# Performance work log

Measured on AMD Instinct MI355X. Metric: run time of the kernel, lower is better.

Reference implementation:

```python
import jax, jax.numpy as jnp
import numpy as np

B, S, D = 2, 2048, 2048
NH, NKV, HD = 16, 4, 128
REP = NH // NKV
EPS = 1e-6
ROPE_THETA = 1e6


def setup_inputs() -> dict:
    key = jax.random.key(0)
    ks = jax.random.split(key, 6)
    x = jax.random.normal(ks[0], (B, S, D), jnp.float32)
    # real rotary embeddings: [S, HD]
    inv_freq = 1.0 / (ROPE_THETA ** (np.arange(0, HD, 2, dtype=np.float64) / HD))
    freqs = np.outer(np.arange(S, dtype=np.float64), inv_freq)
    emb = np.concatenate([freqs, freqs], axis=-1)
    cos = jnp.asarray(np.cos(emb), jnp.float32)
    sin = jnp.asarray(np.sin(emb), jnp.float32)
    scale = 1.0 / np.sqrt(D)
    Wq = jax.random.normal(ks[1], (D, NH * HD), jnp.float32) * scale   # [in, out]
    Wk = jax.random.normal(ks[2], (D, NKV * HD), jnp.float32) * scale
    Wv = jax.random.normal(ks[3], (D, NKV * HD), jnp.float32) * scale
    Wo = jax.random.normal(ks[4], (NH * HD, D), jnp.float32) * (1.0 / np.sqrt(NH * HD))
    q_norm_w = jnp.ones((HD,), jnp.float32)
    k_norm_w = jnp.ones((HD,), jnp.float32)
    return dict(x=x, cos=cos, sin=sin, Wq=Wq, Wk=Wk, Wv=Wv, Wo=Wo,
                q_norm_w=q_norm_w, k_norm_w=k_norm_w)


def _rms_norm(h, w):
    var = jnp.mean(h * h, axis=-1, keepdims=True)
    return w * (h * jax.lax.rsqrt(var + EPS))


def _rotate_half(h):
    h1, h2 = jnp.split(h, 2, axis=-1)
    return jnp.concatenate([-h2, h1], axis=-1)


def reference(x, cos, sin, Wq, Wk, Wv, Wo, q_norm_w, k_norm_w):
    b, s, _ = x.shape
    q = (x @ Wq).reshape(b, s, NH, HD)
    k = (x @ Wk).reshape(b, s, NKV, HD)
    v = (x @ Wv).reshape(b, s, NKV, HD)
    # per-head QK RMSNorm
    q = _rms_norm(q, q_norm_w)
    k = _rms_norm(k, k_norm_w)
    # RoPE: cos/sin [S,HD] -> broadcast over batch and heads
    c = cos[None, :, None, :]
    s_ = sin[None, :, None, :]
    q = q * c + _rotate_half(q) * s_
    k = k * c + _rotate_half(k) * s_
    # GQA: group q heads per kv head instead of materializing repeat_kv
    qg = q.reshape(b, s, NKV, REP, HD)
    scores = jnp.einsum('bqgrd,bkgd->bgrqk', qg, k) / np.sqrt(HD)
    causal = jnp.tril(jnp.ones((s, s), bool))  # [q,k]
    scores = jnp.where(causal, scores, -jnp.inf)
    probs = jax.nn.softmax(scores.astype(jnp.float32), axis=-1).astype(q.dtype)
    out = jnp.einsum('bgrqk,bkgd->bqgrd', probs, v).reshape(b, s, NH * HD)
    return out @ Wo
```

## Files before the change

kernel.cpp:

```cpp
#include <hip/hip_runtime.h>
#include <hip/hip_bf16.h>
#include <math.h>

#define B_ 2
#define S_ 2048
#define D_ 2048
#define NH_ 16
#define NKV_ 4
#define HD_ 128
#define EPS_ 1e-6f
#define SCALE_ 0.08838834764831845f
#define LOG2E_ 1.4426950408889634f
#define KOFF_ 2048
#define VOFF_ 2560

typedef float f32x4 __attribute__((ext_vector_type(4)));
typedef short bf16x8 __attribute__((ext_vector_type(8)));
typedef short short4v __attribute__((ext_vector_type(4)));
typedef float float4v __attribute__((ext_vector_type(4)));
typedef unsigned uint2v __attribute__((ext_vector_type(2)));
typedef unsigned uint4v __attribute__((ext_vector_type(4)));

static __device__ __forceinline__ short f2bf(float f) {
    union { float f; unsigned u; } x{f};
    unsigned r = (x.u + 0x7fff + ((x.u >> 16) & 1)) >> 16;
    return (short)r;
}
static __device__ __forceinline__ float bf2f(short s) {
    union { unsigned u; float f; } x; x.u = ((unsigned)(unsigned short)s) << 16; return x.f;
}
static __device__ __forceinline__ unsigned pack_bf2(float a, float b) {
    return __builtin_amdgcn_perm(__builtin_bit_cast(unsigned, b),
                                 __builtin_bit_cast(unsigned, a), 0x07060302u);
}

#define AS1(p) ((const __attribute__((address_space(1))) void*)(p))
#define AS3(p) ((__attribute__((address_space(3))) void*)(p))
static __device__ __forceinline__ void async16(const void* g, void* l) {
    __builtin_amdgcn_global_load_lds(AS1(g), AS3(l), 16, 0, 0);
}
#define SB_() __builtin_amdgcn_sched_barrier(0)

__global__ __launch_bounds__(256) void cast_kernel(const float* __restrict__ in,
                                                   short* __restrict__ out) {
    size_t i = ((size_t)blockIdx.x * 256 + threadIdx.x) * 4;
    float4v v = *(const float4v*)(in + i);
    short4v o; o.x = f2bf(v.x); o.y = f2bf(v.y); o.z = f2bf(v.z); o.w = f2bf(v.w);
    *(short4v*)(out + i) = o;
}

__global__ __launch_bounds__(256) void transpose_all_kernel(const float* __restrict__ Wq,
                                                            const float* __restrict__ Wk,
                                                            const float* __restrict__ Wv,
                                                            const float* __restrict__ Wo,
                                                            short* __restrict__ Wt,
                                                            short* __restrict__ Wot) {
    __shared__ float tile[64][65];
    const int bx = blockIdx.x, by = blockIdx.y;
    const float* src; short* dst; int N, nb;
    if (bx < 32)      { src = Wq; dst = Wt;                         N = 2048; nb = bx; }
    else if (bx < 40) { src = Wk; dst = Wt + (size_t)KOFF_ * 2048;  N = 512;  nb = bx - 32; }
    else if (bx < 48) { src = Wv; dst = Wt + (size_t)VOFF_ * 2048;  N = 512;  nb = bx - 40; }
    else              { src = Wo; dst = Wot;                        N = 2048; nb = bx - 48; }
    const int n0 = nb * 64, k0 = by * 64;
    const int tid = threadIdx.x;
    for (int r = 0; r < 16; ++r) {
        int k = r * 4 + (tid >> 6);
        int n = tid & 63;
        tile[k][n] = src[(size_t)(k0 + k) * N + n0 + n];
    }
    __syncthreads();
    for (int r = 0; r < 4; ++r) {
        int n  = r * 16 + (tid >> 4);
        int kk = (tid & 15) * 4;
        short4v o4;
        o4.x = f2bf(tile[kk + 0][n]); o4.y = f2bf(tile[kk + 1][n]);
        o4.z = f2bf(tile[kk + 2][n]); o4.w = f2bf(tile[kk + 3][n]);
        *(short4v*)&dst[(size_t)(n0 + n) * 2048 + k0 + kk] = o4;
    }
}

__global__ __launch_bounds__(512, 2) void gemm_oproj_kernel(const short* __restrict__ A,
                                                            const short* __restrict__ Bt,
                                                            float* __restrict__ C) {
    __shared__ __align__(16) short smem[49152];
    short* A0 = smem;
    short* A1 = smem + 8192;
    short* B0 = smem + 16384;
    short* B1 = smem + 32768;

    const int tid  = threadIdx.x;
    const int orig = blockIdx.y * 8 + blockIdx.x;
    const int swz  = (orig & 7) * 32 + (orig >> 3);
    const int bn = swz & 7, bm = swz >> 3;
    const int wave = tid >> 6, lane = tid & 63;
    const int quad = lane >> 4, l16 = lane & 15;
    const int wr = wave >> 2, wc = wave & 3;

    const short* Ag = A  + (size_t)(bm * 128) * 2048;
    const short* Bg = Bt + (size_t)(bn * 256) * 2048;

    f32x4 acc[4][4];
#pragma unroll
    for (int i = 0; i < 4; ++i)
#pragma unroll
        for (int j = 0; j < 4; ++j) acc[i][j] = (f32x4){0.f, 0.f, 0.f, 0.f};

    bf16x8 a[4][2], b0[2][2], b1[2][2];

    auto stage_half = [&](const short* gpanel, int t, int h, short* lslot) {
#pragma unroll
        for (int u = 0; u < 2; ++u) {
            int ci = u * 512 + tid;
            int r  = ci >> 3;
            int cb = ((ci & 7) * 16) ^ ((r & 7) << 4);
            async16(gpanel + (size_t)(h * 128 + r) * 2048 + t * 64 + (cb >> 1),
                    lslot + h * 8192 + ci * 8);
        }
    };

#define OLDA_(lbuf) \
    _Pragma("unroll") for (int mt = 0; mt < 4; ++mt) \
    _Pragma("unroll") for (int ks = 0; ks < 2; ++ks) { \
        int row_ = wr * 64 + mt * 16 + l16; \
        int cb_  = (ks * 64 + quad * 16) ^ ((row_ & 7) << 4); \
        a[mt][ks] = *(const bf16x8*)&(lbuf)[row_ * 64 + (cb_ >> 1)]; \
    }
#define OLDB_(lbuf, qn, breg) \
    _Pragma("unroll") for (int ntl = 0; ntl < 2; ++ntl) \
    _Pragma("unroll") for (int ks = 0; ks < 2; ++ks) { \
        int row_ = wc * 64 + (qn) * 32 + ntl * 16 + l16; \
        int cb_  = (ks * 64 + quad * 16) ^ ((row_ & 7) << 4); \
        breg[ntl][ks] = *(const bf16x8*)&(lbuf)[row_ * 64 + (cb_ >> 1)]; \
    }
#define OBAR_() do { SB_(); __builtin_amdgcn_s_barrier(); } while (0)
#define OMFMA_(qn, breg) do { \
    __builtin_amdgcn_s_setprio(1); \
    _Pragma("unroll") for (int mt = 0; mt < 4; ++mt) \
    _Pragma("unroll") for (int ntl = 0; ntl < 2; ++ntl) \
    _Pragma("unroll") for (int ks = 0; ks < 2; ++ks) \
        acc[mt][(qn) * 2 + ntl] = __builtin_amdgcn_mfma_f32_16x16x32_bf16( \
            a[mt][ks], breg[ntl][ks], acc[mt][(qn) * 2 + ntl], 0, 0, 0); \
    __builtin_amdgcn_s_setprio(0); SB_(); __builtin_amdgcn_s_barrier(); } while (0)

    stage_half(Bg, 0, 0, B0); stage_half(Bg, 0, 1, B0);
    stage_half(Ag, 0, 0, A0);
    SB_(); asm volatile("s_waitcnt vmcnt(0)" ::: "memory");
    __builtin_amdgcn_s_barrier();

#pragma unroll 1
    for (int i = 0; i < 16; ++i) {
        const int tE = 2 * i, tO = 2 * i + 1;
        const bool more = (i < 15);

        stage_half(Ag, tO, 0, A1);
        stage_half(Bg, tO, 0, B1); stage_half(Bg, tO, 1, B1);
        OLDA_(A0); OLDB_(B0, 0, b0);
        OBAR_();
        OMFMA_(0, b0);

        if (more) {
            stage_half(Ag, tE + 2, 0, A0);
            SB_(); asm volatile("s_waitcnt vmcnt(2)" ::: "memory");
        } else {
            SB_(); asm volatile("s_waitcnt vmcnt(0)" ::: "memory");
        }
        OLDB_(B0, 1, b1);
        OBAR_();
        OMFMA_(1, b1);

        if (more) { stage_half(Bg, tE + 2, 0, B0); stage_half(Bg, tE + 2, 1, B0); }
        OLDA_(A1); OLDB_(B1, 0, b0);
        OBAR_();
        OMFMA_(0, b0);

        if (more) { SB_(); asm volatile("s_waitcnt vmcnt(0)" ::: "memory"); }
        OLDB_(B1, 1, b1);
        OBAR_();
        OMFMA_(1, b1);
    }

#pragma unroll
    for (int mt = 0; mt < 4; ++mt)
#pragma unroll
        for (int nt = 0; nt < 4; ++nt)
#pragma unroll
            for (int j = 0; j < 4; ++j) {
                int row = bm * 128 + wr * 64 + mt * 16 + quad * 4 + j;
                int col = bn * 256 + wc * 64 + nt * 16 + l16;
                C[(size_t)row * 2048 + col] = acc[mt][nt][j];
            }
#undef OLDA_
#undef OLDB_
#undef OBAR_
#undef OMFMA_
}

#define QKV_ITERS 16

__global__ __launch_bounds__(512, 2) void qkv_fused_kernel(const short* __restrict__ xb,
                                                           const short* __restrict__ Wt,
                                                           const float* __restrict__ cosb,
                                                           const float* __restrict__ sinb,
                                                           const float* __restrict__ qw,
                                                           const float* __restrict__ kw,
                                                           short* __restrict__ q_rope,
                                                           short* __restrict__ k_rope,
                                                           short* __restrict__ vtr) {
    __shared__ __align__(16) short smem[65536];
    __shared__ float ss2[4][256];

    short* A0 = smem;
    short* A1 = smem + 16384;
    short* B0 = smem + 32768;
    short* B1 = smem + 49152;

    const int tid  = threadIdx.x;
    const int orig = blockIdx.y * 12 + blockIdx.x;
    const int swz  = (orig & 7) * 24 + (orig >> 3);
    const int bn = swz % 12, bm = swz / 12;
    const int wave = tid >> 6, lane = tid & 63;
    const int quad = lane >> 4, l16 = lane & 15;
    const int wr = wave >> 2, wc = wave & 3;

    const short* Ag = xb + (size_t)(bm * 256) * 2048;
    const short* Bg = Wt + (size_t)(bn * 256) * 2048;

    f32x4 acc[8][4];
#pragma unroll
    for (int i = 0; i < 8; ++i)
#pragma unroll
        for (int j = 0; j < 4; ++j) acc[i][j] = (f32x4){0.f, 0.f, 0.f, 0.f};

    bf16x8 a[4][2], b0[2][2], b1[2][2];

    auto stage_half = [&](const short* gpanel, int t, int h, short* lslot) {
#pragma unroll
        for (int u = 0; u < 2; ++u) {
            int ci = u * 512 + tid;
            int r  = ci >> 3;
            int cb = ((ci & 7) * 16) ^ ((r & 7) << 4);
            async16(gpanel + (size_t)(h * 128 + r) * 2048 + t * 64 + (cb >> 1),
                    lslot + h * 8192 + ci * 8);
        }
    };

#define LDA_(lbuf, qm) \
    _Pragma("unroll") for (int mt = 0; mt < 4; ++mt) \
    _Pragma("unroll") for (int ks = 0; ks < 2; ++ks) { \
        int row_ = wr * 128 + (qm) * 64 + mt * 16 + l16; \
        int cb_  = (ks * 64 + quad * 16) ^ ((row_ & 7) << 4); \
        a[mt][ks] = *(const bf16x8*)&(lbuf)[row_ * 64 + (cb_ >> 1)]; \
    }
#define LDB_(lbuf, qn, breg) \
    _Pragma("unroll") for (int ntl = 0; ntl < 2; ++ntl) \
    _Pragma("unroll") for (int ks = 0; ks < 2; ++ks) { \
        int row_ = wc * 64 + (qn) * 32 + ntl * 16 + l16; \
        int cb_  = (ks * 64 + quad * 16) ^ ((row_ & 7) << 4); \
        breg[ntl][ks] = *(const bf16x8*)&(lbuf)[row_ * 64 + (cb_ >> 1)]; \
    }
#define MFMA16_(qm, qn, breg) \
    _Pragma("unroll") for (int mt = 0; mt < 4; ++mt) \
    _Pragma("unroll") for (int ntl = 0; ntl < 2; ++ntl) \
    _Pragma("unroll") for (int ks = 0; ks < 2; ++ks) \
        acc[(qm) * 4 + mt][(qn) * 2 + ntl] = __builtin_amdgcn_mfma_f32_16x16x32_bf16( \
            a[mt][ks], breg[ntl][ks], acc[(qm) * 4 + mt][(qn) * 2 + ntl], 0, 0, 0);
#define PH_BAR() do { __builtin_amdgcn_sched_barrier(0); __builtin_amdgcn_s_barrier(); } while (0)
#define PH_MFMA2(qm) do { \
        __builtin_amdgcn_s_setprio(1); MFMA16_(qm, 0, b0); MFMA16_(qm, 1, b1); \
        __builtin_amdgcn_s_setprio(0); \
        __builtin_amdgcn_sched_barrier(0); __builtin_amdgcn_s_barrier(); } while (0)

    stage_half(Bg, 0, 0, B0); stage_half(Bg, 0, 1, B0);
    stage_half(Ag, 0, 0, A0); stage_half(Ag, 0, 1, A0);
    stage_half(Bg, 1, 0, B1); stage_half(Bg, 1, 1, B1);
    asm volatile("s_waitcnt vmcnt(4)" ::: "memory");
    __builtin_amdgcn_s_barrier();

#pragma unroll 1
    for (int i = 0; i < QKV_ITERS; ++i) {
        const int tE = 2 * i, tO = 2 * i + 1;
        const bool more = (i < QKV_ITERS - 1);

        LDA_(A0, 0); LDB_(B0, 0, b0); LDB_(B0, 1, b1);
        stage_half(Ag, tO, 0, A1); stage_half(Ag, tO, 1, A1);
        PH_BAR();
        PH_MFMA2(0);

        LDA_(A0, 1);
        if (more) {
            stage_half(Bg, tE + 2, 0, B0); stage_half(Bg, tE + 2, 1, B0);
            asm volatile("s_waitcnt vmcnt(4)" ::: "memory");
        } else {
            asm volatile("s_waitcnt vmcnt(0)" ::: "memory");
        }
        PH_BAR();
        PH_MFMA2(1);

        LDA_(A1, 0); LDB_(B1, 0, b0); LDB_(B1, 1, b1);
        if (more) { stage_half(Ag, tE + 2, 0, A0); stage_half(Ag, tE + 2, 1, A0); }
        PH_BAR();
        PH_MFMA2(0);

        LDA_(A1, 1);
        if (more) {
            stage_half(Bg, tO + 2, 0, B1); stage_half(Bg, tO + 2, 1, B1);
            asm volatile("s_waitcnt vmcnt(4)" ::: "memory");
        }
        PH_BAR();
        PH_MFMA2(1);
    }

    if (bn >= 10) {
        const int gbase = (bn - 10) * 2;
#pragma unroll
        for (int am = 0; am < 8; ++am) {
            int tok0 = bm * 256 + wr * 128 + am * 16 + quad * 4;
            int bb = tok0 >> 11, s0 = tok0 & (S_ - 1);
#pragma unroll
            for (int nt = 0; nt < 4; ++nt) {
                int col = wc * 64 + nt * 16 + l16;
                int g = gbase + (col >> 7);
                int d = col & 127;
                short4v o4;
                o4.x = f2bf(acc[am][nt][0]); o4.y = f2bf(acc[am][nt][1]);
                o4.z = f2bf(acc[am][nt][2]); o4.w = f2bf(acc[am][nt][3]);
                *(short4v*)&vtr[((size_t)(bb * NKV_ + g) * HD_ + d) * S_ + s0] = o4;
            }
        }
        return;
    }

    {
        float pss[8][4];
#pragma unroll
        for (int am = 0; am < 8; ++am)
#pragma unroll
            for (int j = 0; j < 4; ++j) {
                float s = 0.f;
#pragma unroll
                for (int nt = 0; nt < 4; ++nt) s += acc[am][nt][j] * acc[am][nt][j];
                pss[am][j] = s;
            }
#pragma unroll
        for (int off = 1; off < 16; off <<= 1)
#pragma unroll
            for (int am = 0; am < 8; ++am)
#pragma unroll
                for (int j = 0; j < 4; ++j)
                    pss[am][j] += __shfl_xor(pss[am][j], off);
        if (l16 == 0)
#pragma unroll
            for (int am = 0; am < 8; ++am)
#pragma unroll
                for (int j = 0; j < 4; ++j)
                    ss2[wc][wr * 128 + am * 16 + quad * 4 + j] = pss[am][j];
    }
    short* ct = smem;
#pragma unroll
    for (int am = 0; am < 8; ++am)
#pragma unroll
        for (int nt = 0; nt < 4; ++nt)
#pragma unroll
            for (int j = 0; j < 4; ++j)
                ct[(wr * 128 + am * 16 + quad * 4 + j) * 256 + wc * 64 + nt * 16 + l16]
                    = f2bf(acc[am][nt][j]);
    __syncthreads();

    const bool isQ = (bn < 8);
    const float osc = isQ ? (SCALE_ * LOG2E_) : 1.0f;
    const float* w = isQ ? qw : kw;
#pragma unroll 1
    for (int it = 0; it < 16; ++it) {
        int idx = it * 512 + tid;
        int row = idx >> 5;
        int s32 = idx & 31;
        int head = s32 >> 4, seg = s32 & 15;
        int tok = bm * 256 + row;
        int bb = tok >> 11, s = tok & (S_ - 1);
        float rstd = rsqrtf((ss2[2 * head][row] + ss2[2 * head + 1][row]) * (1.0f / HD_) + EPS_);
        int c0 = seg * 8, p0 = (seg ^ 8) * 8;
        bf16x8 ta = *(const bf16x8*)&ct[row * 256 + head * 128 + c0];
        bf16x8 tb = *(const bf16x8*)&ct[row * 256 + head * 128 + p0];
        float sgn = (seg < 8) ? -1.0f : 1.0f;
        float4v cs0 = *(const float4v*)&cosb[(size_t)s * HD_ + c0];
        float4v cs1 = *(const float4v*)&cosb[(size_t)s * HD_ + c0 + 4];
        float4v sn0 = *(const float4v*)&sinb[(size_t)s * HD_ + c0];
        float4v sn1 = *(const float4v*)&sinb[(size_t)s * HD_ + c0 + 4];
        float ov[8];
#pragma unroll
        for (int i = 0; i < 8; ++i) {
            float n1 = bf2f(ta[i]) * rstd * w[c0 + i];
            float n2 = bf2f(tb[i]) * rstd * w[p0 + i];
            float cs = (i < 4) ? cs0[i & 3] : cs1[i & 3];
            float sn = (i < 4) ? sn0[i & 3] : sn1[i & 3];
            ov[i] = (n1 * cs + sgn * n2 * sn) * osc;
        }
        uint4v wv;
#pragma unroll
        for (int i2 = 0; i2 < 4; ++i2)
            wv[i2] = ((unsigned)(unsigned short)f2bf(ov[2 * i2])) |
                     ((unsigned)(unsigned short)f2bf(ov[2 * i2 + 1]) << 16);
        int gh = isQ ? (bn * 2 + head) : ((bn - 8) * 2 + head);
        short* dst = isQ
            ? q_rope + ((size_t)(bb * S_ + s) * NH_ + gh) * HD_ + c0
            : k_rope + ((size_t)(bb * NKV_ + gh) * S_ + s) * HD_ + c0;
        *(uint4v*)dst = wv;
    }
#undef LDA_
#undef LDB_
#undef MFMA16_
#undef PH_BAR
#undef PH_MFMA2
}

__global__ __launch_bounds__(256, 1) void attn_kernel(const short* __restrict__ qr,
                                                      const short* __restrict__ kg,
                                                      const short* __restrict__ vt,
                                                      short* __restrict__ aout) {
    __shared__ short Ks[2][64 * 128];
    __shared__ short Vs[2][128 * 64];

    const int lin = blockIdx.x;
    const int b  = lin & 1;
    const int g  = (lin >> 1) & 3;
    const int hq = (lin >> 3) & 3;
    const int pr = lin >> 5;
    const int h  = g * 4 + hq;

    const int wave = threadIdx.x >> 6, lane = threadIdx.x & 63;
    const int quad = lane >> 4, l16 = lane & 15;

    const short* kbase = kg + (size_t)(b * NKV_ + g) * S_ * HD_;
    const short* vbase = vt + (size_t)(b * NKV_ + g) * HD_ * S_;

    for (int pass = 0; pass < 2; ++pass) {
        const int qt    = pass ? (15 - pr) : pr;
        const int iters = 2 * qt + 2;
        int qrow0 = qt * 128 + wave * 16 + l16;
        int qrow1 = qrow0 + 64;

        bf16x8 qf[2][4];
#pragma unroll
        for (int qs = 0; qs < 2; ++qs) {
            const short* qp = qr + ((size_t)(b * S_ + (qs ? qrow1 : qrow0)) * NH_ + h) * HD_;
#pragma unroll
            for (int ks = 0; ks < 4; ++ks)
                qf[qs][ks] = *(const bf16x8*)(qp + ks * 32 + quad * 8);
        }

        f32x4 o[2][8];
#pragma unroll
        for (int qs = 0; qs < 2; ++qs)
#pragma unroll
            for (int i = 0; i < 8; ++i) o[qs][i] = (f32x4){0.f, 0.f, 0.f, 0.f};
        float m_i[2] = {-INFINITY, -INFINITY};
        float l_i[2] = {0.f, 0.f};

        auto stage = [&](int kt, int bsel) {
            const short* kt_base = kbase + (size_t)kt * 64 * HD_;
            const short* vt_base = vbase + kt * 64;
            for (int t = 0; t < 4; ++t) {
                int ci  = (wave * 4 + t) * 64 + lane;
                int key = ci >> 4;
                int c   = (ci & 15) ^ ((key ^ (key >> 2)) & 15);
                async16(kt_base + key * HD_ + c * 8, &Ks[bsel][ci * 8]);
            }
            for (int t = 0; t < 4; ++t) {
                int ci = (wave * 4 + t) * 64 + lane;
                int d  = ci >> 3;
                int c  = (ci & 7) ^ (d & 7);
                async16(vt_base + (size_t)d * S_ + c * 8, &Vs[bsel][ci * 8]);
            }
        };

        stage(0, 0);
        int buf = 0;
        for (int kt = 0; kt < iters; ++kt) {
            __syncthreads();
            if (kt + 1 < iters) stage(kt + 1, buf ^ 1);

            f32x4 acc[2][4];
#pragma unroll
            for (int qs = 0; qs < 2; ++qs)
#pragma unroll
                for (int t = 0; t < 4; ++t) acc[qs][t] = (f32x4){0.f, 0.f, 0.f, 0.f};
            __builtin_amdgcn_s_setprio(1);
#pragma unroll
            for (int t = 0; t < 4; ++t) {
                int lk = ((t >> 1) << 5) + ((l16 >> 2) << 3) + ((t & 1) << 2) + (l16 & 3);
                const short* kp = &Ks[buf][lk * 128];
                int pm = (lk ^ (lk >> 2)) & 15;
#pragma unroll
                for (int ks = 0; ks < 4; ++ks) {
                    bf16x8 kf = *(const bf16x8*)(kp + (((ks * 4 + quad) ^ pm) * 8));
                    acc[0][t] = __builtin_amdgcn_mfma_f32_16x16x32_bf16(kf, qf[0][ks], acc[0][t], 0, 0, 0);
                    acc[1][t] = __builtin_amdgcn_mfma_f32_16x16x32_bf16(kf, qf[1][ks], acc[1][t], 0, 0, 0);
                }
            }
            __builtin_amdgcn_s_setprio(0);
            const int key_base = kt * 64;
#pragma unroll
            for (int qs = 0; qs < 2; ++qs) {
                int qmin = qt * 128 + qs * 64 + wave * 16;
                int qrow = qs ? qrow1 : qrow0;
                if (key_base + 63 > qmin) {
#pragma unroll
                    for (int t = 0; t < 4; ++t)
#pragma unroll
                        for (int j = 0; j < 4; ++j) {
                            int kl = key_base + ((t >> 1) << 5) + (quad << 3) + ((t & 1) << 2) + j;
                            if (kl > qrow) acc[qs][t][j] = -INFINITY;
                        }
                }
            }
            unsigned pk[2][2][4];
#pragma unroll
            for (int qs = 0; qs < 2; ++qs) {
                float mx = m_i[qs];
#pragma unroll
                for (int t = 0; t < 4; ++t)
#pragma unroll
                    for (int j = 0; j < 4; ++j) mx = fmaxf(mx, acc[qs][t][j]);
                mx = fmaxf(mx, __shfl_xor(mx, 16));
                mx = fmaxf(mx, __shfl_xor(mx, 32));
                float al = __builtin_amdgcn_exp2f(m_i[qs] - mx);
                m_i[qs] = mx;
                float rs = 0.f;
                float p[4][4];
#pragma unroll
                for (int t = 0; t < 4; ++t)
#pragma unroll
                    for (int j = 0; j < 4; ++j) {
                        float e = __builtin_amdgcn_exp2f(acc[qs][t][j] - mx);
                        p[t][j] = e;
                        rs += e;
                    }
                rs += __shfl_xor(rs, 16);
                rs += __shfl_xor(rs, 32);
                l_i[qs] = al * l_i[qs] + rs;
#pragma unroll
                for (int d8 = 0; d8 < 8; ++d8)
#pragma unroll
                    for (int j = 0; j < 4; ++j) o[qs][d8][j] *= al;
#pragma unroll
                for (int grp = 0; grp < 2; ++grp) {
                    pk[qs][grp][0] = pack_bf2(p[2 * grp][0],     p[2 * grp][1]);
                    pk[qs][grp][1] = pack_bf2(p[2 * grp][2],     p[2 * grp][3]);
                    pk[qs][grp][2] = pack_bf2(p[2 * grp + 1][0], p[2 * grp + 1][1]);
                    pk[qs][grp][3] = pack_bf2(p[2 * grp + 1][2], p[2 * grp + 1][3]);
                }
            }
            __builtin_amdgcn_s_setprio(1);
#pragma unroll
            for (int grp = 0; grp < 2; ++grp) {
                union { unsigned u[4]; bf16x8 v; } pb0, pb1;
#pragma unroll
                for (int i = 0; i < 4; ++i) { pb0.u[i] = pk[0][grp][i]; pb1.u[i] = pk[1][grp][i]; }
#pragma unroll
                for (int d8 = 0; d8 < 8; ++d8) {
                    int d = d8 * 16 + l16;
                    bf16x8 vf = *(const bf16x8*)&Vs[buf][d * 64 + (((grp * 4 + quad) ^ (d & 7)) * 8)];
                    o[0][d8] = __builtin_amdgcn_mfma_f32_16x16x32_bf16(vf, pb0.v, o[0][d8], 0, 0, 0);
                    o[1][d8] = __builtin_amdgcn_mfma_f32_16x16x32_bf16(vf, pb1.v, o[1][d8], 0, 0, 0);
                }
            }
            __builtin_amdgcn_s_setprio(0);
            buf ^= 1;
        }
#pragma unroll
        for (int qs = 0; qs < 2; ++qs) {
            float il = 1.0f / l_i[qs];
            int qrow = qs ? qrow1 : qrow0;
            short* op = aout + ((size_t)(b * S_ + qrow) * NH_ + h) * HD_ + quad * 4;
#pragma unroll
            for (int d8 = 0; d8 < 8; ++d8) {
                uint2v wv;
                wv.x = ((unsigned)(unsigned short)f2bf(o[qs][d8][0] * il)) |
                       ((unsigned)(unsigned short)f2bf(o[qs][d8][1] * il) << 16);
                wv.y = ((unsigned)(unsigned short)f2bf(o[qs][d8][2] * il)) |
                       ((unsigned)(unsigned short)f2bf(o[qs][d8][3] * il) << 16);
                *(uint2v*)(op + d8 * 16) = wv;
            }
        }
        __syncthreads();
    }
}

extern "C" void kernel_launch(void* const* d_in, const int* in_sizes, int n_in,
                              void* d_out, int out_size, void* d_ws, size_t ws_size,
                              hipStream_t stream) {
    (void)in_sizes; (void)n_in; (void)out_size; (void)ws_size;
    const float* x    = (const float*)d_in[0];
    const float* cosb = (const float*)d_in[1];
    const float* sinb = (const float*)d_in[2];
    const float* Wq   = (const float*)d_in[3];
    const float* Wk   = (const float*)d_in[4];
    const float* Wv   = (const float*)d_in[5];
    const float* Wo   = (const float*)d_in[6];
    const float* qw   = (const float*)d_in[7];
    const float* kw   = (const float*)d_in[8];
    float* out = (float*)d_out;

    char* ws = (char*)d_ws;
    short* xb     = (short*)ws;  ws += (size_t)4096 * 2048 * 2;
    short* Wt     = (short*)ws;  ws += (size_t)3072 * 2048 * 2;
    short* Wot    = (short*)ws;  ws += (size_t)2048 * 2048 * 2;
    short* q_rope = (short*)ws;  ws += (size_t)4096 * 2048 * 2;
    short* k_rope = (short*)ws;  ws += (size_t)4096 * 512 * 2;
    short* vt     = (short*)ws;  ws += (size_t)4096 * 512 * 2;
    short* a_out  = (short*)ws;  ws += (size_t)4096 * 2048 * 2;

    const int M = B_ * S_;

    cast_kernel<<<M * 2048 / 1024, 256, 0, stream>>>(x, xb);
    transpose_all_kernel<<<dim3(80, 32), 256, 0, stream>>>(Wq, Wk, Wv, Wo, Wt, Wot);

    qkv_fused_kernel<<<dim3(12, M / 256), 512, 0, stream>>>(
        xb, Wt, cosb, sinb, qw, kw, q_rope, k_rope, vt);

    attn_kernel<<<256, 256, 0, stream>>>(q_rope, k_rope, vt, a_out);

    gemm_oproj_kernel<<<dim3(8, 32), 512, 0, stream>>>(a_out, Wot, out);
}
```

Before: 312.5 us.

## Split attention KV loop across two wave groups with LDS merge of partial softmax

The attention kernel grows to 512 threads, and two groups of four waves each process alternating 64-key tiles for the same 128-query tile. This halves the serial KV iterations per wave and doubles waves per CU to hide latency. At the end, the partial outputs, maxima and sums are exchanged through LDS and merged flash-decoding style. In exchange it uses twice the LDS, adds an extra merge and barriers, and changes the -inf initialisation to a finite value so the merge stays free of NaNs.

```diff
diff --git a/kernel.cpp b/kernel.cpp
--- a/kernel.cpp
+++ b/kernel.cpp
@@ -13,6 +13,7 @@
 #define LOG2E_ 1.4426950408889634f
 #define KOFF_ 2048
 #define VOFF_ 2560
+#define MINIT_ -1e30f
 
 typedef float f32x4 __attribute__((ext_vector_type(4)));
 typedef short bf16x8 __attribute__((ext_vector_type(8)));
@@ -414,12 +415,12 @@
 #undef PH_MFMA2
 }
 
-__global__ __launch_bounds__(256, 1) void attn_kernel(const short* __restrict__ qr,
+__global__ __launch_bounds__(512, 1) void attn_kernel(const short* __restrict__ qr,
                                                       const short* __restrict__ kg,
                                                       const short* __restrict__ vt,
                                                       short* __restrict__ aout) {
-    __shared__ short Ks[2][64 * 128];
-    __shared__ short Vs[2][128 * 64];
+    __shared__ __align__(16) short Ks[2][2][8192];
+    __shared__ __align__(16) short Vs[2][2][8192];
 
     const int lin = blockIdx.x;
     const int b  = lin & 1;
@@ -430,15 +431,37 @@
 
     const int wave = threadIdx.x >> 6, lane = threadIdx.x & 63;
     const int quad = lane >> 4, l16 = lane & 15;
+    const int half = wave >> 2;
+    const int ww   = wave & 3;
 
     const short* kbase = kg + (size_t)(b * NKV_ + g) * S_ * HD_;
     const short* vbase = vt + (size_t)(b * NKV_ + g) * HD_ * S_;
 
-    for (int pass = 0; pass < 2; ++pass) {
-        const int qt    = pass ? (15 - pr) : pr;
-        const int iters = 2 * qt + 2;
-        int qrow0 = qt * 128 + wave * 16 + l16;
-        int qrow1 = qrow0 + 64;
+    auto stage = [&](int kt, short* Kd, short* Vd) {
+        const short* kt_base = kbase + (size_t)kt * 64 * HD_;
+        const short* vt_base = vbase + kt * 64;
+#pragma unroll
+        for (int t = 0; t < 2; ++t) {
+            int ci  = (wave * 2 + t) * 64 + lane;
+            int key = ci >> 4;
+            int c   = (ci & 15) ^ ((key ^ (key >> 2)) & 15);
+            async16(kt_base + key * HD_ + c * 8, Kd + ci * 8);
+        }
+#pragma unroll
+        for (int t = 0; t < 2; ++t) {
+            int ci = (wave * 2 + t) * 64 + lane;
+            int d  = ci >> 3;
+            int c  = (ci & 7) ^ (d & 7);
+            async16(vt_base + (size_t)d * S_ + c * 8, Vd + ci * 8);
+        }
+    };
+
+#pragma unroll 1
+    for (int ph = 0; ph < 2; ++ph) {
+        const int qt    = ph ? (15 - pr) : pr;
+        const int nhalf = qt + 1;
+        const int qrow0 = qt * 128 + ww * 16 + l16;
+        const int qrow1 = qrow0 + 64;
 
         bf16x8 qf[2][4];
 #pragma unroll
@@ -454,31 +477,22 @@
         for (int qs = 0; qs < 2; ++qs)
 #pragma unroll
             for (int i = 0; i < 8; ++i) o[qs][i] = (f32x4){0.f, 0.f, 0.f, 0.f};
-        float m_i[2] = {-INFINITY, -INFINITY};
+        float m_i[2] = {MINIT_, MINIT_};
         float l_i[2] = {0.f, 0.f};
 
-        auto stage = [&](int kt, int bsel) {
-            const short* kt_base = kbase + (size_t)kt * 64 * HD_;
-            const short* vt_base = vbase + kt * 64;
-            for (int t = 0; t < 4; ++t) {
-                int ci  = (wave * 4 + t) * 64 + lane;
-                int key = ci >> 4;
-                int c   = (ci & 15) ^ ((key ^ (key >> 2)) & 15);
-                async16(kt_base + key * HD_ + c * 8, &Ks[bsel][ci * 8]);
-            }
-            for (int t = 0; t < 4; ++t) {
-                int ci = (wave * 4 + t) * 64 + lane;
-                int d  = ci >> 3;
-                int c  = (ci & 7) ^ (d & 7);
-                async16(vt_base + (size_t)d * S_ + c * 8, &Vs[bsel][ci * 8]);
-            }
-        };
-
-        stage(0, 0);
+        stage(0, Ks[0][0], Vs[0][0]);
+        stage(1, Ks[1][0], Vs[1][0]);
         int buf = 0;
-        for (int kt = 0; kt < iters; ++kt) {
+#pragma unroll 1
+        for (int i = 0; i < nhalf; ++i) {
             __syncthreads();
-            if (kt + 1 < iters) stage(kt + 1, buf ^ 1);
+            if (i + 1 < nhalf) {
+                stage(2 * i + 2, Ks[0][buf ^ 1], Vs[0][buf ^ 1]);
+                stage(2 * i + 3, Ks[1][buf ^ 1], Vs[1][buf ^ 1]);
+            }
+            const short* Kb = Ks[half][buf];
+            const short* Vb = Vs[half][buf];
+            const int ktm = 2 * i + half;
 
             f32x4 acc[2][4];
 #pragma unroll
@@ -489,7 +503,7 @@
 #pragma unroll
             for (int t = 0; t < 4; ++t) {
                 int lk = ((t >> 1) << 5) + ((l16 >> 2) << 3) + ((t & 1) << 2) + (l16 & 3);
-                const short* kp = &Ks[buf][lk * 128];
+                const short* kp = &Kb[lk * 128];
                 int pm = (lk ^ (lk >> 2)) & 15;
 #pragma unroll
                 for (int ks = 0; ks < 4; ++ks) {
@@ -499,10 +513,10 @@
                 }
             }
             __builtin_amdgcn_s_setprio(0);
-            const int key_base = kt * 64;
+            const int key_base = ktm * 64;
 #pragma unroll
             for (int qs = 0; qs < 2; ++qs) {
-                int qmin = qt * 128 + qs * 64 + wave * 16;
+                int qmin = qt * 128 + qs * 64 + ww * 16;
                 int qrow = qs ? qrow1 : qrow0;
                 if (key_base + 63 > qmin) {
 #pragma unroll
@@ -556,11 +570,11 @@
             for (int grp = 0; grp < 2; ++grp) {
                 union { unsigned u[4]; bf16x8 v; } pb0, pb1;
 #pragma unroll
-                for (int i = 0; i < 4; ++i) { pb0.u[i] = pk[0][grp][i]; pb1.u[i] = pk[1][grp][i]; }
+                for (int i2 = 0; i2 < 4; ++i2) { pb0.u[i2] = pk[0][grp][i2]; pb1.u[i2] = pk[1][grp][i2]; }
 #pragma unroll
                 for (int d8 = 0; d8 < 8; ++d8) {
                     int d = d8 * 16 + l16;
-                    bf16x8 vf = *(const bf16x8*)&Vs[buf][d * 64 + (((grp * 4 + quad) ^ (d & 7)) * 8)];
+                    bf16x8 vf = *(const bf16x8*)&Vb[d * 64 + (((grp * 4 + quad) ^ (d & 7)) * 8)];
                     o[0][d8] = __builtin_amdgcn_mfma_f32_16x16x32_bf16(vf, pb0.v, o[0][d8], 0, 0, 0);
                     o[1][d8] = __builtin_amdgcn_mfma_f32_16x16x32_bf16(vf, pb1.v, o[1][d8], 0, 0, 0);
                 }
@@ -568,19 +582,46 @@
             __builtin_amdgcn_s_setprio(0);
             buf ^= 1;
         }
-#pragma unroll
-        for (int qs = 0; qs < 2; ++qs) {
-            float il = 1.0f / l_i[qs];
-            int qrow = qs ? qrow1 : qrow0;
-            short* op = aout + ((size_t)(b * S_ + qrow) * NH_ + h) * HD_ + quad * 4;
-#pragma unroll
-            for (int d8 = 0; d8 < 8; ++d8) {
-                uint2v wv;
-                wv.x = ((unsigned)(unsigned short)f2bf(o[qs][d8][0] * il)) |
-                       ((unsigned)(unsigned short)f2bf(o[qs][d8][1] * il) << 16);
-                wv.y = ((unsigned)(unsigned short)f2bf(o[qs][d8][2] * il)) |
-                       ((unsigned)(unsigned short)f2bf(o[qs][d8][3] * il) << 16);
-                *(uint2v*)(op + d8 * 16) = wv;
+
+        __syncthreads();
+        float* exch = (float*)(ww < 2 ? &Ks[0][0][0] : &Vs[0][0][0]);
+        float* slot = exch + ((size_t)((ww & 1) * 64 + lane) * 68);
+        if (half == 1) {
+#pragma unroll
+            for (int qs = 0; qs < 2; ++qs) {
+#pragma unroll
+                for (int d8 = 0; d8 < 8; ++d8)
+#pragma unroll
+                    for (int j = 0; j < 4; ++j)
+                        slot[qs * 32 + d8 * 4 + j] = o[qs][d8][j];
+                slot[64 + qs] = m_i[qs];
+                slot[66 + qs] = l_i[qs];
+            }
+        }
+        __syncthreads();
+        if (half == 0) {
+#pragma unroll
+            for (int qs = 0; qs < 2; ++qs) {
+                float mB = slot[64 + qs], lB = slot[66 + qs];
+                float m  = fmaxf(m_i[qs], mB);
+                float wA = __builtin_amdgcn_exp2f(m_i[qs] - m);
+                float wB = __builtin_amdgcn_exp2f(mB - m);
+                float il = 1.0f / (l_i[qs] * wA + lB * wB);
+                int qrow = qs ? qrow1 : qrow0;
+                short* op = aout + ((size_t)(b * S_ + qrow) * NH_ + h) * HD_ + quad * 4;
+#pragma unroll
+                for (int d8 = 0; d8 < 8; ++d8) {
+                    float v0 = (o[qs][d8][0] * wA + slot[qs * 32 + d8 * 4 + 0] * wB) * il;
+                    float v1 = (o[qs][d8][1] * wA + slot[qs * 32 + d8 * 4 + 1] * wB) * il;
+                    float v2 = (o[qs][d8][2] * wA + slot[qs * 32 + d8 * 4 + 2] * wB) * il;
+                    float v3 = (o[qs][d8][3] * wA + slot[qs * 32 + d8 * 4 + 3] * wB) * il;
+                    uint2v wv;
+                    wv.x = ((unsigned)(unsigned short)f2bf(v0)) |
+                           ((unsigned)(unsigned short)f2bf(v1) << 16);
+                    wv.y = ((unsigned)(unsigned short)f2bf(v2)) |
+                           ((unsigned)(unsigned short)f2bf(v3) << 16);
+                    *(uint2v*)(op + d8 * 16) = wv;
+                }
             }
         }
         __syncthreads();
@@ -619,7 +660,7 @@
     qkv_fused_kernel<<<dim3(12, M / 256), 512, 0, stream>>>(
         xb, Wt, cosb, sinb, qw, kw, q_rope, k_rope, vt);
 
-    attn_kernel<<<256, 256, 0, stream>>>(q_rope, k_rope, vt, a_out);
+    attn_kernel<<<256, 512, 0, stream>>>(q_rope, k_rope, vt, a_out);
 
     gemm_oproj_kernel<<<dim3(8, 32), 512, 0, stream>>>(a_out, Wot, out);
 }
```

After: 286.6 us. 8.3% less time.
